# Optimization experiments

Measured on AMD Instinct MI355X. Metric: run time of the kernel, lower is better.

The kernel has to match this reference:

```python
import jax, jax.numpy as jnp
import numpy as np

NUM_HEADS = 8
DIM = 256  # == out_dim; module implicitly requires dim == out_dim


def setup_inputs() -> dict:
    key = jax.random.key(0)
    k0, k1, k2, k3, k4, k5 = jax.random.split(key, 6)
    B, N, T, dim = 4, 128, 128, DIM
    s = dim ** -0.5
    return {
        "v": jax.random.normal(k0, (B, N, T, dim), dtype=jnp.float32),
        "Wq": jax.random.normal(k1, (dim, dim), dtype=jnp.float32) * s,
        "Wk": jax.random.normal(k2, (dim, dim), dtype=jnp.float32) * s,
        "Wv": jax.random.normal(k3, (dim, dim), dtype=jnp.float32) * s,
        "Wp": jax.random.normal(k4, (dim, dim), dtype=jnp.float32) * s,
        "bp": jax.random.normal(k5, (dim,), dtype=jnp.float32) * 0.01,
    }


def reference(v, Wq, Wk, Wv, Wp, bp):
    B, N, T, dim = v.shape
    H = NUM_HEADS
    hd = dim // H
    scale = hd ** -0.5
    # projections (qkv_bias=False)
    q = (v @ Wq).reshape(B * N, T, H, hd)
    k = (v @ Wk).reshape(B * N, T, H, hd)
    vv = (v @ Wv).reshape(B * N, T, H, hd)
    # NOTE: heads axis is NOT moved before the matmul in the original torch
    # code, so attention is over the HEADS axis: per (b*n, t) an HxH matrix.
    attn = jnp.einsum('mthd,mtgd->mthg', q, k) * scale  # [B*N, T, H, H]
    attn = jax.nn.softmax(attn, axis=-1)
    x = jnp.einsum('mthg,mtgd->mthd', attn, vv).reshape(B, N, T, dim)
    # output projection (with bias); dropout probs are 0 / eval mode
    return x @ Wp + bp
```

## Files before the change

### kernel.cpp

```cpp
#include <hip/hip_runtime.h>
#include <hip/hip_bf16.h>
#include <math.h>


#define DIMX      256
#define NH        8
#define HD        32
#define TM        32
#define NTHREADS  512
#define QSTRIDE   776
#define KT        8
#define NT_QKV    48

typedef _Float16 f16x8 __attribute__((ext_vector_type(8)));
typedef _Float16 f16x4 __attribute__((ext_vector_type(4)));
typedef _Float16 f16x2 __attribute__((ext_vector_type(2)));
typedef float    f32x4 __attribute__((ext_vector_type(4)));

static __device__ __forceinline__ f16x2 pkrtz(float a, float b) {
    return (f16x2)__builtin_amdgcn_cvt_pkrtz(a, b);
}

__global__ void pack_weights(const float* __restrict__ Wq,
                             const float* __restrict__ Wk,
                             const float* __restrict__ Wv,
                             const float* __restrict__ Wp,
                             _Float16* __restrict__ pk)
{
    const int QKV_FRAGS = NT_QKV * KT * 64;
    int u = blockIdx.x * blockDim.x + threadIdx.x;
    const float* W;
    int nt, kt, lane;
    if (u < QKV_FRAGS) {
        nt = u / (KT * 64); kt = (u / 64) % KT; lane = u % 64;
        if (nt < 16)      { W = Wq; }
        else if (nt < 32) { W = Wk; nt -= 16; }
        else              { W = Wv; nt -= 32; }
    } else {
        int u2 = u - QKV_FRAGS;
        nt = u2 / (KT * 64); kt = (u2 / 64) % KT; lane = u2 % 64;
        W = Wp;
    }
    const int n  = nt * 16 + (lane & 15);
    const int k0 = kt * 32 + (lane >> 4) * 8;
    f16x8 frag;
#pragma unroll
    for (int j = 0; j < 8; ++j)
        frag[j] = (_Float16)W[(size_t)(k0 + j) * DIMX + n];
    *(f16x8*)(pk + (size_t)u * 8) = frag;
}

__global__ __launch_bounds__(NTHREADS, 6)
void fused_attn_mfma(const float* __restrict__ v,
                     const _Float16* __restrict__ Wqkv_pk,
                     const _Float16* __restrict__ Wp_pk,
                     const float* __restrict__ bp,
                     float* __restrict__ out)
{
    __shared__ __align__(16) _Float16 S[TM * QSTRIDE];

    const int tid   = threadIdx.x;
    const int lane  = tid & 63;
    const int wv_id = tid >> 6;
    const int l15   = lane & 15;
    const int quad  = lane >> 4;
    const long token0 = (long)blockIdx.x * TM;

    {
        const float4* src = (const float4*)(v + token0 * DIMX);
#pragma unroll
        for (int i = 0; i < 4; ++i) {
            int u = tid + NTHREADS * i;
            int m = u >> 6;
            int c = (u & 63) * 4;
            float4 t4 = src[u];
            f16x2 lo = pkrtz(t4.x, t4.y), hi = pkrtz(t4.z, t4.w);
            f16x4 b4 = { lo.x, lo.y, hi.x, hi.y };
            *(f16x4*)&S[m * QSTRIDE + c] = b4;
        }
    }
    __syncthreads();

    f32x4 acc1[2][3];
    int tiles1[3] = { 2 * wv_id, 2 * wv_id + 1, 40 + wv_id };
    {
        int tiles0[3] = { 16 + wv_id * 3, 17 + wv_id * 3, 18 + wv_id * 3 };

        f32x4 acc0[2][3];
#pragma unroll
        for (int tt = 0; tt < 2; ++tt)
#pragma unroll
            for (int j = 0; j < 3; ++j)
                acc0[tt][j] = (f32x4){0.f, 0.f, 0.f, 0.f};
        {
            const f16x8* wb = (const f16x8*)Wqkv_pk + lane;
            f16x8 wcur[3];
#pragma unroll
            for (int j = 0; j < 3; ++j)
                wcur[j] = wb[(size_t)(tiles0[j] * KT) * 64];
            for (int kt = 0; kt < KT; ++kt) {
                const int ktn = (kt + 1 < KT) ? kt + 1 : KT - 1;
                f16x8 wnxt[3];
#pragma unroll
                for (int j = 0; j < 3; ++j)
                    wnxt[j] = wb[(size_t)(tiles0[j] * KT + ktn) * 64];
                f16x8 vf[2];
#pragma unroll
                for (int tt = 0; tt < 2; ++tt)
                    vf[tt] = *(const f16x8*)&S[(tt * 16 + l15) * QSTRIDE + kt * 32 + quad * 8];
#pragma unroll
                for (int j = 0; j < 3; ++j) {
                    acc0[0][j] = __builtin_amdgcn_mfma_f32_16x16x32_f16(wcur[j], vf[0], acc0[0][j], 0, 0, 0);
                    acc0[1][j] = __builtin_amdgcn_mfma_f32_16x16x32_f16(wcur[j], vf[1], acc0[1][j], 0, 0, 0);
                }
#pragma unroll
                for (int j = 0; j < 3; ++j) wcur[j] = wnxt[j];
            }
        }
#pragma unroll
        for (int tt = 0; tt < 2; ++tt)
#pragma unroll
            for (int j = 0; j < 3; ++j) {
                f16x2 a = pkrtz(acc0[tt][j][0], acc0[tt][j][1]);
                f16x2 b = pkrtz(acc0[tt][j][2], acc0[tt][j][3]);
                f16x4 p4 = { a.x, a.y, b.x, b.y };
                *(f16x4*)&S[(tt * 16 + l15) * QSTRIDE + tiles0[j] * 16 + quad * 4] = p4;
            }

#pragma unroll
        for (int tt = 0; tt < 2; ++tt)
#pragma unroll
            for (int j = 0; j < 3; ++j)
                acc1[tt][j] = (f32x4){0.f, 0.f, 0.f, 0.f};
        {
            const f16x8* wb = (const f16x8*)Wqkv_pk + lane;
            f16x8 wcur[3];
#pragma unroll
            for (int j = 0; j < 3; ++j)
                wcur[j] = wb[(size_t)(tiles1[j] * KT) * 64];
            for (int kt = 0; kt < KT; ++kt) {
                const int ktn = (kt + 1 < KT) ? kt + 1 : KT - 1;
                f16x8 wnxt[3];
#pragma unroll
                for (int j = 0; j < 3; ++j)
                    wnxt[j] = wb[(size_t)(tiles1[j] * KT + ktn) * 64];
                f16x8 vf[2];
#pragma unroll
                for (int tt = 0; tt < 2; ++tt)
                    vf[tt] = *(const f16x8*)&S[(tt * 16 + l15) * QSTRIDE + kt * 32 + quad * 8];
#pragma unroll
                for (int j = 0; j < 3; ++j) {
                    acc1[0][j] = __builtin_amdgcn_mfma_f32_16x16x32_f16(wcur[j], vf[0], acc1[0][j], 0, 0, 0);
                    acc1[1][j] = __builtin_amdgcn_mfma_f32_16x16x32_f16(wcur[j], vf[1], acc1[1][j], 0, 0, 0);
                }
#pragma unroll
                for (int j = 0; j < 3; ++j) wcur[j] = wnxt[j];
            }
        }
    }
    __syncthreads();

#pragma unroll
    for (int tt = 0; tt < 2; ++tt)
#pragma unroll
        for (int j = 0; j < 3; ++j) {
            f16x2 a = pkrtz(acc1[tt][j][0], acc1[tt][j][1]);
            f16x2 b = pkrtz(acc1[tt][j][2], acc1[tt][j][3]);
            f16x4 p4 = { a.x, a.y, b.x, b.y };
            *(f16x4*)&S[(tt * 16 + l15) * QSTRIDE + tiles1[j] * 16 + quad * 4] = p4;
        }
    __syncthreads();

    {
        const int ta  = tid >> 4;
        const int sub = tid & 15;
        const int h   = sub >> 1;
        const int d0  = (sub & 1) * 16;
        const float scale = 0.17677669529663687f;

        const _Float16* qrow  = &S[ta * QSTRIDE + h * HD + d0];
        const _Float16* kbase = &S[ta * QSTRIDE + 256 + d0];
        const _Float16* vbase = &S[ta * QSTRIDE + 512 + d0];

        f16x8 q0 = *(const f16x8*)qrow;
        f16x8 q1 = *(const f16x8*)(qrow + 8);

        float logits[NH];
#pragma unroll
        for (int g = 0; g < NH; ++g) {
            f16x8 k0 = *(const f16x8*)(kbase + g * HD);
            f16x8 k1 = *(const f16x8*)(kbase + g * HD + 8);
            f16x8 p  = q0 * k0;
            p += q1 * k1;
            f16x4 r4 = __builtin_shufflevector(p, p, 0, 1, 2, 3)
                     + __builtin_shufflevector(p, p, 4, 5, 6, 7);
            f16x2 r2 = __builtin_shufflevector(r4, r4, 0, 1)
                     + __builtin_shufflevector(r4, r4, 2, 3);
            logits[g] = (float)r2.x + (float)r2.y;
        }
#pragma unroll
        for (int g = 0; g < NH; ++g)
            logits[g] = (logits[g] + __shfl_xor(logits[g], 1, 64)) * scale;

        float mx = logits[0];
#pragma unroll
        for (int g = 1; g < NH; ++g) mx = fmaxf(mx, logits[g]);
        float se = 0.f;
#pragma unroll
        for (int g = 0; g < NH; ++g) { logits[g] = __expf(logits[g] - mx); se += logits[g]; }
        float inv = 1.f / se;

        f16x8 xa0 = (f16x8)(_Float16)0.f;
        f16x8 xa1 = (f16x8)(_Float16)0.f;
#pragma unroll
        for (int g = 0; g < NH; ++g) {
            _Float16 ph = (_Float16)(logits[g] * inv);
            f16x8 pw = { ph, ph, ph, ph, ph, ph, ph, ph };
            f16x8 v0 = *(const f16x8*)(vbase + g * HD);
            f16x8 v1 = *(const f16x8*)(vbase + g * HD + 8);
            xa0 += pw * v0;
            xa1 += pw * v1;
        }
        __syncthreads();
        *(f16x8*)&S[ta * QSTRIDE + h * HD + d0]     = xa0;
        *(f16x8*)&S[ta * QSTRIDE + h * HD + d0 + 8] = xa1;
    }
    __syncthreads();

    {
        const int nt0 = wv_id * 2;
        f32x4 acc[2][2];
#pragma unroll
        for (int tt = 0; tt < 2; ++tt)
#pragma unroll
            for (int j = 0; j < 2; ++j)
                acc[tt][j] = (f32x4){0.f, 0.f, 0.f, 0.f};

        const f16x8* wb = (const f16x8*)Wp_pk + lane;
        f16x8 wcur[2];
#pragma unroll
        for (int j = 0; j < 2; ++j)
            wcur[j] = wb[(size_t)((nt0 + j) * KT) * 64];

        for (int kt = 0; kt < KT; ++kt) {
            const int ktn = (kt + 1 < KT) ? kt + 1 : KT - 1;
            f16x8 wnxt[2];
#pragma unroll
            for (int j = 0; j < 2; ++j)
                wnxt[j] = wb[(size_t)((nt0 + j) * KT + ktn) * 64];
            f16x8 xf[2];
#pragma unroll
            for (int tt = 0; tt < 2; ++tt)
                xf[tt] = *(const f16x8*)&S[(tt * 16 + l15) * QSTRIDE + kt * 32 + quad * 8];
#pragma unroll
            for (int j = 0; j < 2; ++j) {
                acc[0][j] = __builtin_amdgcn_mfma_f32_16x16x32_f16(wcur[j], xf[0], acc[0][j], 0, 0, 0);
                acc[1][j] = __builtin_amdgcn_mfma_f32_16x16x32_f16(wcur[j], xf[1], acc[1][j], 0, 0, 0);
            }
#pragma unroll
            for (int j = 0; j < 2; ++j) wcur[j] = wnxt[j];
        }
#pragma unroll
        for (int j = 0; j < 2; ++j) {
            f32x4 b = *(const f32x4*)&bp[(nt0 + j) * 16 + quad * 4];
#pragma unroll
            for (int tt = 0; tt < 2; ++tt) {
                f32x4 o = acc[tt][j] + b;
                *(f32x4*)&out[(token0 + tt * 16 + l15) * DIMX + (nt0 + j) * 16 + quad * 4] = o;
            }
        }
    }
}

extern "C" void kernel_launch(void* const* d_in, const int* in_sizes, int n_in,
                              void* d_out, int out_size, void* d_ws, size_t ws_size,
                              hipStream_t stream) {
    const float* v  = (const float*)d_in[0];
    const float* Wq = (const float*)d_in[1];
    const float* Wk = (const float*)d_in[2];
    const float* Wv = (const float*)d_in[3];
    const float* Wp = (const float*)d_in[4];
    const float* bp = (const float*)d_in[5];
    float* out = (float*)d_out;

    _Float16* pk = (_Float16*)d_ws;
    const _Float16* Wqkv_pk = pk;
    const _Float16* Wp_pk   = pk + (size_t)24576 * 8;

    pack_weights<<<256, 128, 0, stream>>>(Wq, Wk, Wv, Wp, pk);

    const int ntokens = in_sizes[0] / DIMX;
    fused_attn_mfma<<<ntokens / TM, NTHREADS, 0, stream>>>(v, Wqkv_pk, Wp_pk, bp, out);
}
```

Before: 158.7 us.

## Cache activations in registers and deepen weight prefetch ring for QKV and proj GEMMs

The input tile fragments are loaded from LDS into registers once and reused across all six QKV output tiles. Writes of Q/K/V results to shared memory can then go in place without the two-phase split and its extra barrier. Weight fragments are streamed through an 8-deep register ring (4-deep for the output projection), with Wp prefetch hoisted before the attention stage. The global loads of v and the first weights are also issued before the fp16 conversion. This trades more registers for fewer LDS reads and more latency hiding, and occupancy bounds drop from 6 to 4 waves per SIMD.

```diff
diff --git a/kernel.cpp b/kernel.cpp
--- a/kernel.cpp
+++ b/kernel.cpp
@@ -50,7 +50,7 @@
     *(f16x8*)(pk + (size_t)u * 8) = frag;
 }
 
-__global__ __launch_bounds__(NTHREADS, 6)
+__global__ __launch_bounds__(NTHREADS, 4)
 void fused_attn_mfma(const float* __restrict__ v,
                      const _Float16* __restrict__ Wqkv_pk,
                      const _Float16* __restrict__ Wp_pk,
@@ -66,109 +66,72 @@
     const int quad  = lane >> 4;
     const long token0 = (long)blockIdx.x * TM;
 
-    {
-        const float4* src = (const float4*)(v + token0 * DIMX);
-#pragma unroll
-        for (int i = 0; i < 4; ++i) {
-            int u = tid + NTHREADS * i;
-            int m = u >> 6;
-            int c = (u & 63) * 4;
-            float4 t4 = src[u];
-            f16x2 lo = pkrtz(t4.x, t4.y), hi = pkrtz(t4.z, t4.w);
-            f16x4 b4 = { lo.x, lo.y, hi.x, hi.y };
-            *(f16x4*)&S[m * QSTRIDE + c] = b4;
-        }
-    }
-    __syncthreads();
-
-    f32x4 acc1[2][3];
-    int tiles1[3] = { 2 * wv_id, 2 * wv_id + 1, 40 + wv_id };
-    {
-        int tiles0[3] = { 16 + wv_id * 3, 17 + wv_id * 3, 18 + wv_id * 3 };
-
-        f32x4 acc0[2][3];
-#pragma unroll
-        for (int tt = 0; tt < 2; ++tt)
-#pragma unroll
-            for (int j = 0; j < 3; ++j)
-                acc0[tt][j] = (f32x4){0.f, 0.f, 0.f, 0.f};
-        {
-            const f16x8* wb = (const f16x8*)Wqkv_pk + lane;
-            f16x8 wcur[3];
-#pragma unroll
-            for (int j = 0; j < 3; ++j)
-                wcur[j] = wb[(size_t)(tiles0[j] * KT) * 64];
-            for (int kt = 0; kt < KT; ++kt) {
-                const int ktn = (kt + 1 < KT) ? kt + 1 : KT - 1;
-                f16x8 wnxt[3];
-#pragma unroll
-                for (int j = 0; j < 3; ++j)
-                    wnxt[j] = wb[(size_t)(tiles0[j] * KT + ktn) * 64];
-                f16x8 vf[2];
-#pragma unroll
-                for (int tt = 0; tt < 2; ++tt)
-                    vf[tt] = *(const f16x8*)&S[(tt * 16 + l15) * QSTRIDE + kt * 32 + quad * 8];
-#pragma unroll
-                for (int j = 0; j < 3; ++j) {
-                    acc0[0][j] = __builtin_amdgcn_mfma_f32_16x16x32_f16(wcur[j], vf[0], acc0[0][j], 0, 0, 0);
-                    acc0[1][j] = __builtin_amdgcn_mfma_f32_16x16x32_f16(wcur[j], vf[1], acc0[1][j], 0, 0, 0);
-                }
-#pragma unroll
-                for (int j = 0; j < 3; ++j) wcur[j] = wnxt[j];
+    const int tiles[6] = { 16 + wv_id * 3, 17 + wv_id * 3, 18 + wv_id * 3,
+                           2 * wv_id, 2 * wv_id + 1, 40 + wv_id };
+
+    const float4* src = (const float4*)(v + token0 * DIMX);
+    float4 t4[4];
+#pragma unroll
+    for (int i = 0; i < 4; ++i)
+        t4[i] = src[tid + NTHREADS * i];
+
+    const f16x8* wb = (const f16x8*)Wqkv_pk + lane;
+    f16x8 Wr[8];
+#pragma unroll
+    for (int p = 0; p < 8; ++p)
+        Wr[p] = wb[(size_t)(tiles[0] * KT + p) * 64];
+
+#pragma unroll
+    for (int i = 0; i < 4; ++i) {
+        int u = tid + NTHREADS * i;
+        int m = u >> 6;
+        int c = (u & 63) * 4;
+        f16x2 lo = pkrtz(t4[i].x, t4[i].y), hi = pkrtz(t4[i].z, t4[i].w);
+        f16x4 b4 = { lo.x, lo.y, hi.x, hi.y };
+        *(f16x4*)&S[m * QSTRIDE + c] = b4;
+    }
+    __syncthreads();
+
+    f16x8 vr[2][KT];
+#pragma unroll
+    for (int tt = 0; tt < 2; ++tt)
+#pragma unroll
+        for (int kt = 0; kt < KT; ++kt)
+            vr[tt][kt] = *(const f16x8*)&S[(tt * 16 + l15) * QSTRIDE + kt * 32 + quad * 8];
+    __syncthreads();
+
+#pragma unroll
+    for (int j = 0; j < 6; ++j) {
+        f32x4 acc[2];
+        acc[0] = (f32x4){0.f, 0.f, 0.f, 0.f};
+        acc[1] = (f32x4){0.f, 0.f, 0.f, 0.f};
+#pragma unroll
+        for (int kt = 0; kt < KT; ++kt) {
+            const int u = j * KT + kt;
+            f16x8 w = Wr[u & 7];
+            if (u + 8 < 6 * KT) {
+                const int un = u + 8;
+                Wr[u & 7] = wb[(size_t)(tiles[un >> 3] * KT + (un & 7)) * 64];
             }
-        }
-#pragma unroll
-        for (int tt = 0; tt < 2; ++tt)
-#pragma unroll
-            for (int j = 0; j < 3; ++j) {
-                f16x2 a = pkrtz(acc0[tt][j][0], acc0[tt][j][1]);
-                f16x2 b = pkrtz(acc0[tt][j][2], acc0[tt][j][3]);
-                f16x4 p4 = { a.x, a.y, b.x, b.y };
-                *(f16x4*)&S[(tt * 16 + l15) * QSTRIDE + tiles0[j] * 16 + quad * 4] = p4;
-            }
-
-#pragma unroll
-        for (int tt = 0; tt < 2; ++tt)
-#pragma unroll
-            for (int j = 0; j < 3; ++j)
-                acc1[tt][j] = (f32x4){0.f, 0.f, 0.f, 0.f};
-        {
-            const f16x8* wb = (const f16x8*)Wqkv_pk + lane;
-            f16x8 wcur[3];
-#pragma unroll
-            for (int j = 0; j < 3; ++j)
-                wcur[j] = wb[(size_t)(tiles1[j] * KT) * 64];
-            for (int kt = 0; kt < KT; ++kt) {
-                const int ktn = (kt + 1 < KT) ? kt + 1 : KT - 1;
-                f16x8 wnxt[3];
-#pragma unroll
-                for (int j = 0; j < 3; ++j)
-                    wnxt[j] = wb[(size_t)(tiles1[j] * KT + ktn) * 64];
-                f16x8 vf[2];
-#pragma unroll
-                for (int tt = 0; tt < 2; ++tt)
-                    vf[tt] = *(const f16x8*)&S[(tt * 16 + l15) * QSTRIDE + kt * 32 + quad * 8];
-#pragma unroll
-                for (int j = 0; j < 3; ++j) {
-                    acc1[0][j] = __builtin_amdgcn_mfma_f32_16x16x32_f16(wcur[j], vf[0], acc1[0][j], 0, 0, 0);
-                    acc1[1][j] = __builtin_amdgcn_mfma_f32_16x16x32_f16(wcur[j], vf[1], acc1[1][j], 0, 0, 0);
-                }
-#pragma unroll
-                for (int j = 0; j < 3; ++j) wcur[j] = wnxt[j];
-            }
-        }
-    }
-    __syncthreads();
-
-#pragma unroll
-    for (int tt = 0; tt < 2; ++tt)
-#pragma unroll
-        for (int j = 0; j < 3; ++j) {
-            f16x2 a = pkrtz(acc1[tt][j][0], acc1[tt][j][1]);
-            f16x2 b = pkrtz(acc1[tt][j][2], acc1[tt][j][3]);
+            acc[0] = __builtin_amdgcn_mfma_f32_16x16x32_f16(w, vr[0][kt], acc[0], 0, 0, 0);
+            acc[1] = __builtin_amdgcn_mfma_f32_16x16x32_f16(w, vr[1][kt], acc[1], 0, 0, 0);
+        }
+#pragma unroll
+        for (int tt = 0; tt < 2; ++tt) {
+            f16x2 a = pkrtz(acc[tt][0], acc[tt][1]);
+            f16x2 b = pkrtz(acc[tt][2], acc[tt][3]);
             f16x4 p4 = { a.x, a.y, b.x, b.y };
-            *(f16x4*)&S[(tt * 16 + l15) * QSTRIDE + tiles1[j] * 16 + quad * 4] = p4;
-        }
+            *(f16x4*)&S[(tt * 16 + l15) * QSTRIDE + tiles[j] * 16 + quad * 4] = p4;
+        }
+    }
+
+    const f16x8* wb2 = (const f16x8*)Wp_pk + lane;
+    const int nt0 = wv_id * 2;
+    f16x8 W2[4];
+#pragma unroll
+    for (int p = 0; p < 4; ++p)
+        W2[p] = wb2[(size_t)((nt0 + (p & 1)) * KT + (p >> 1)) * 64];
+
     __syncthreads();
 
     {
@@ -228,7 +191,6 @@
     __syncthreads();
 
     {
-        const int nt0 = wv_id * 2;
         f32x4 acc[2][2];
 #pragma unroll
         for (int tt = 0; tt < 2; ++tt)
@@ -236,29 +198,21 @@
             for (int j = 0; j < 2; ++j)
                 acc[tt][j] = (f32x4){0.f, 0.f, 0.f, 0.f};
 
-        const f16x8* wb = (const f16x8*)Wp_pk + lane;
-        f16x8 wcur[2];
-#pragma unroll
-        for (int j = 0; j < 2; ++j)
-            wcur[j] = wb[(size_t)((nt0 + j) * KT) * 64];
-
+#pragma unroll
         for (int kt = 0; kt < KT; ++kt) {
-            const int ktn = (kt + 1 < KT) ? kt + 1 : KT - 1;
-            f16x8 wnxt[2];
-#pragma unroll
-            for (int j = 0; j < 2; ++j)
-                wnxt[j] = wb[(size_t)((nt0 + j) * KT + ktn) * 64];
             f16x8 xf[2];
 #pragma unroll
             for (int tt = 0; tt < 2; ++tt)
                 xf[tt] = *(const f16x8*)&S[(tt * 16 + l15) * QSTRIDE + kt * 32 + quad * 8];
 #pragma unroll
             for (int j = 0; j < 2; ++j) {
-                acc[0][j] = __builtin_amdgcn_mfma_f32_16x16x32_f16(wcur[j], xf[0], acc[0][j], 0, 0, 0);
-                acc[1][j] = __builtin_amdgcn_mfma_f32_16x16x32_f16(wcur[j], xf[1], acc[1][j], 0, 0, 0);
+                const int u = kt * 2 + j;
+                f16x8 w = W2[u & 3];
+                if (u + 4 < 2 * KT)
+                    W2[u & 3] = wb2[(size_t)((nt0 + j) * KT + (kt + 2)) * 64];
+                acc[0][j] = __builtin_amdgcn_mfma_f32_16x16x32_f16(w, xf[0], acc[0][j], 0, 0, 0);
+                acc[1][j] = __builtin_amdgcn_mfma_f32_16x16x32_f16(w, xf[1], acc[1][j], 0, 0, 0);
             }
-#pragma unroll
-            for (int j = 0; j < 2; ++j) wcur[j] = wnxt[j];
         }
 #pragma unroll
         for (int j = 0; j < 2; ++j) {
```

Result: slower. 254.4 us (+60.3%).

## Enlarge token tile to 48 with deeper weight prefetch and per-head attention threads

Applied to the files above, without the earlier changes.

Raises the per-block token tile from 32 to 48 rows so each weight fragment loaded from global memory feeds three MFMA row tiles instead of two. Adds a two-stage register prefetch of the weight fragments in the fully unrolled k-loops. Reworks the attention phase so each thread handles a whole head without a shuffle reduction, and adds bounds handling for a partial last block. Lowers the launch-bounds occupancy hint from 6 to 2 and uses more LDS per block, which reduces how many blocks fit per CU and leaves some threads idle during attention.

```diff
diff --git a/kernel.cpp b/kernel.cpp
--- a/kernel.cpp
+++ b/kernel.cpp
@@ -6,7 +6,7 @@
 #define DIMX      256
 #define NH        8
 #define HD        32
-#define TM        32
+#define TM        48
 #define NTHREADS  512
 #define QSTRIDE   776
 #define KT        8
@@ -50,12 +50,13 @@
     *(f16x8*)(pk + (size_t)u * 8) = frag;
 }
 
-__global__ __launch_bounds__(NTHREADS, 6)
+__global__ __launch_bounds__(NTHREADS, 2)
 void fused_attn_mfma(const float* __restrict__ v,
                      const _Float16* __restrict__ Wqkv_pk,
                      const _Float16* __restrict__ Wp_pk,
                      const float* __restrict__ bp,
-                     float* __restrict__ out)
+                     float* __restrict__ out,
+                     int ntok)
 {
     __shared__ __align__(16) _Float16 S[TM * QSTRIDE];
 
@@ -64,144 +65,167 @@
     const int wv_id = tid >> 6;
     const int l15   = lane & 15;
     const int quad  = lane >> 4;
-    const long token0 = (long)blockIdx.x * TM;
+    const int token0 = blockIdx.x * TM;
+    int valid = ntok - token0; if (valid > TM) valid = TM;
+
+    const int tiles0[3] = { 16 + 3 * wv_id, 17 + 3 * wv_id, 18 + 3 * wv_id };
+    const int tiles1[3] = { 2 * wv_id, 2 * wv_id + 1, 40 + wv_id };
+
+    const f16x8* wb  = (const f16x8*)Wqkv_pk + lane;
+    const f16x8* wb2 = (const f16x8*)Wp_pk + lane;
 
     {
-        const float4* src = (const float4*)(v + token0 * DIMX);
-#pragma unroll
-        for (int i = 0; i < 4; ++i) {
+        const float4* src = (const float4*)(v + (size_t)token0 * DIMX);
+        float4 t4[6];
+#pragma unroll
+        for (int i = 0; i < 6; ++i) {
+            int u = tid + NTHREADS * i;
+            int m = u >> 6;
+            t4[i] = (m < valid) ? src[u] : (float4){0.f, 0.f, 0.f, 0.f};
+        }
+#pragma unroll
+        for (int i = 0; i < 6; ++i) {
             int u = tid + NTHREADS * i;
             int m = u >> 6;
             int c = (u & 63) * 4;
-            float4 t4 = src[u];
-            f16x2 lo = pkrtz(t4.x, t4.y), hi = pkrtz(t4.z, t4.w);
+            f16x2 lo = pkrtz(t4[i].x, t4[i].y), hi = pkrtz(t4[i].z, t4[i].w);
             f16x4 b4 = { lo.x, lo.y, hi.x, hi.y };
             *(f16x4*)&S[m * QSTRIDE + c] = b4;
         }
     }
-    __syncthreads();
-
-    f32x4 acc1[2][3];
-    int tiles1[3] = { 2 * wv_id, 2 * wv_id + 1, 40 + wv_id };
-    {
-        int tiles0[3] = { 16 + wv_id * 3, 17 + wv_id * 3, 18 + wv_id * 3 };
-
-        f32x4 acc0[2][3];
-#pragma unroll
-        for (int tt = 0; tt < 2; ++tt)
+    f16x8 wA[3], wB[3];
+#pragma unroll
+    for (int j = 0; j < 3; ++j) wA[j] = wb[(size_t)(tiles0[j] * KT + 0) * 64];
+#pragma unroll
+    for (int j = 0; j < 3; ++j) wB[j] = wb[(size_t)(tiles0[j] * KT + 1) * 64];
+    __syncthreads();
+
+    f32x4 acc0[3][3];
+#pragma unroll
+    for (int j = 0; j < 3; ++j)
+#pragma unroll
+        for (int tt = 0; tt < 3; ++tt)
+            acc0[j][tt] = (f32x4){0.f, 0.f, 0.f, 0.f};
+
+#pragma unroll
+    for (int kt = 0; kt < KT; ++kt) {
+        f16x8 wC[3];
+        if (kt < KT - 2) {
 #pragma unroll
             for (int j = 0; j < 3; ++j)
-                acc0[tt][j] = (f32x4){0.f, 0.f, 0.f, 0.f};
-        {
-            const f16x8* wb = (const f16x8*)Wqkv_pk + lane;
-            f16x8 wcur[3];
+                wC[j] = wb[(size_t)(tiles0[j] * KT + kt + 2) * 64];
+        } else {
+#pragma unroll
+            for (int j = 0; j < 3; ++j) wC[j] = wB[j];
+        }
+        f16x8 vf[3];
+#pragma unroll
+        for (int tt = 0; tt < 3; ++tt)
+            vf[tt] = *(const f16x8*)&S[(tt * 16 + l15) * QSTRIDE + kt * 32 + quad * 8];
+#pragma unroll
+        for (int j = 0; j < 3; ++j)
+#pragma unroll
+            for (int tt = 0; tt < 3; ++tt)
+                acc0[j][tt] = __builtin_amdgcn_mfma_f32_16x16x32_f16(wA[j], vf[tt], acc0[j][tt], 0, 0, 0);
+#pragma unroll
+        for (int j = 0; j < 3; ++j) { wA[j] = wB[j]; wB[j] = wC[j]; }
+    }
+
+    f16x8 pA[3], pB[3];
+#pragma unroll
+    for (int j = 0; j < 3; ++j) pA[j] = wb[(size_t)(tiles1[j] * KT + 0) * 64];
+#pragma unroll
+    for (int j = 0; j < 3; ++j) pB[j] = wb[(size_t)(tiles1[j] * KT + 1) * 64];
+
+#pragma unroll
+    for (int j = 0; j < 3; ++j)
+#pragma unroll
+        for (int tt = 0; tt < 3; ++tt) {
+            f16x2 a = pkrtz(acc0[j][tt][0], acc0[j][tt][1]);
+            f16x2 b = pkrtz(acc0[j][tt][2], acc0[j][tt][3]);
+            f16x4 p4 = { a.x, a.y, b.x, b.y };
+            *(f16x4*)&S[(tt * 16 + l15) * QSTRIDE + tiles0[j] * 16 + quad * 4] = p4;
+        }
+
+    f32x4 acc1[3][3];
+#pragma unroll
+    for (int j = 0; j < 3; ++j)
+#pragma unroll
+        for (int tt = 0; tt < 3; ++tt)
+            acc1[j][tt] = (f32x4){0.f, 0.f, 0.f, 0.f};
+
+#pragma unroll
+    for (int kt = 0; kt < KT; ++kt) {
+        f16x8 pC[3];
+        if (kt < KT - 2) {
 #pragma unroll
             for (int j = 0; j < 3; ++j)
-                wcur[j] = wb[(size_t)(tiles0[j] * KT) * 64];
-            for (int kt = 0; kt < KT; ++kt) {
-                const int ktn = (kt + 1 < KT) ? kt + 1 : KT - 1;
-                f16x8 wnxt[3];
-#pragma unroll
-                for (int j = 0; j < 3; ++j)
-                    wnxt[j] = wb[(size_t)(tiles0[j] * KT + ktn) * 64];
-                f16x8 vf[2];
-#pragma unroll
-                for (int tt = 0; tt < 2; ++tt)
-                    vf[tt] = *(const f16x8*)&S[(tt * 16 + l15) * QSTRIDE + kt * 32 + quad * 8];
-#pragma unroll
-                for (int j = 0; j < 3; ++j) {
-                    acc0[0][j] = __builtin_amdgcn_mfma_f32_16x16x32_f16(wcur[j], vf[0], acc0[0][j], 0, 0, 0);
-                    acc0[1][j] = __builtin_amdgcn_mfma_f32_16x16x32_f16(wcur[j], vf[1], acc0[1][j], 0, 0, 0);
-                }
-#pragma unroll
-                for (int j = 0; j < 3; ++j) wcur[j] = wnxt[j];
-            }
-        }
-#pragma unroll
-        for (int tt = 0; tt < 2; ++tt)
-#pragma unroll
-            for (int j = 0; j < 3; ++j) {
-                f16x2 a = pkrtz(acc0[tt][j][0], acc0[tt][j][1]);
-                f16x2 b = pkrtz(acc0[tt][j][2], acc0[tt][j][3]);
-                f16x4 p4 = { a.x, a.y, b.x, b.y };
-                *(f16x4*)&S[(tt * 16 + l15) * QSTRIDE + tiles0[j] * 16 + quad * 4] = p4;
-            }
-
-#pragma unroll
-        for (int tt = 0; tt < 2; ++tt)
-#pragma unroll
-            for (int j = 0; j < 3; ++j)
-                acc1[tt][j] = (f32x4){0.f, 0.f, 0.f, 0.f};
-        {
-            const f16x8* wb = (const f16x8*)Wqkv_pk + lane;
-            f16x8 wcur[3];
-#pragma unroll
-            for (int j = 0; j < 3; ++j)
-                wcur[j] = wb[(size_t)(tiles1[j] * KT) * 64];
-            for (int kt = 0; kt < KT; ++kt) {
-                const int ktn = (kt + 1 < KT) ? kt + 1 : KT - 1;
-                f16x8 wnxt[3];
-#pragma unroll
-                for (int j = 0; j < 3; ++j)
-                    wnxt[j] = wb[(size_t)(tiles1[j] * KT + ktn) * 64];
-                f16x8 vf[2];
-#pragma unroll
-                for (int tt = 0; tt < 2; ++tt)
-                    vf[tt] = *(const f16x8*)&S[(tt * 16 + l15) * QSTRIDE + kt * 32 + quad * 8];
-#pragma unroll
-                for (int j = 0; j < 3; ++j) {
-                    acc1[0][j] = __builtin_amdgcn_mfma_f32_16x16x32_f16(wcur[j], vf[0], acc1[0][j], 0, 0, 0);
-                    acc1[1][j] = __builtin_amdgcn_mfma_f32_16x16x32_f16(wcur[j], vf[1], acc1[1][j], 0, 0, 0);
-                }
-#pragma unroll
-                for (int j = 0; j < 3; ++j) wcur[j] = wnxt[j];
-            }
-        }
-    }
-    __syncthreads();
-
-#pragma unroll
-    for (int tt = 0; tt < 2; ++tt)
-#pragma unroll
-        for (int j = 0; j < 3; ++j) {
-            f16x2 a = pkrtz(acc1[tt][j][0], acc1[tt][j][1]);
-            f16x2 b = pkrtz(acc1[tt][j][2], acc1[tt][j][3]);
+                pC[j] = wb[(size_t)(tiles1[j] * KT + kt + 2) * 64];
+        } else {
+#pragma unroll
+            for (int j = 0; j < 3; ++j) pC[j] = pB[j];
+        }
+        f16x8 vf[3];
+#pragma unroll
+        for (int tt = 0; tt < 3; ++tt)
+            vf[tt] = *(const f16x8*)&S[(tt * 16 + l15) * QSTRIDE + kt * 32 + quad * 8];
+#pragma unroll
+        for (int j = 0; j < 3; ++j)
+#pragma unroll
+            for (int tt = 0; tt < 3; ++tt)
+                acc1[j][tt] = __builtin_amdgcn_mfma_f32_16x16x32_f16(pA[j], vf[tt], acc1[j][tt], 0, 0, 0);
+#pragma unroll
+        for (int j = 0; j < 3; ++j) { pA[j] = pB[j]; pB[j] = pC[j]; }
+    }
+    __syncthreads();
+
+#pragma unroll
+    for (int j = 0; j < 3; ++j)
+#pragma unroll
+        for (int tt = 0; tt < 3; ++tt) {
+            f16x2 a = pkrtz(acc1[j][tt][0], acc1[j][tt][1]);
+            f16x2 b = pkrtz(acc1[j][tt][2], acc1[j][tt][3]);
             f16x4 p4 = { a.x, a.y, b.x, b.y };
             *(f16x4*)&S[(tt * 16 + l15) * QSTRIDE + tiles1[j] * 16 + quad * 4] = p4;
         }
-    __syncthreads();
-
-    {
-        const int ta  = tid >> 4;
-        const int sub = tid & 15;
-        const int h   = sub >> 1;
-        const int d0  = (sub & 1) * 16;
+
+    const int nt0 = 2 * wv_id;
+    f16x8 wA2[2], wB2[2];
+#pragma unroll
+    for (int j = 0; j < 2; ++j) wA2[j] = wb2[(size_t)((nt0 + j) * KT + 0) * 64];
+#pragma unroll
+    for (int j = 0; j < 2; ++j) wB2[j] = wb2[(size_t)((nt0 + j) * KT + 1) * 64];
+    __syncthreads();
+
+    const int ta  = tid >> 3;
+    const int h   = tid & 7;
+    const bool act = (ta < TM);
+    f16x8 xa0, xa1, xa2, xa3;
+    if (act) {
         const float scale = 0.17677669529663687f;
-
-        const _Float16* qrow  = &S[ta * QSTRIDE + h * HD + d0];
-        const _Float16* kbase = &S[ta * QSTRIDE + 256 + d0];
-        const _Float16* vbase = &S[ta * QSTRIDE + 512 + d0];
-
-        f16x8 q0 = *(const f16x8*)qrow;
+        const _Float16* qrow  = &S[ta * QSTRIDE + h * HD];
+        const _Float16* kbase = &S[ta * QSTRIDE + 256];
+        const _Float16* vbase = &S[ta * QSTRIDE + 512];
+
+        f16x8 q0 = *(const f16x8*)(qrow);
         f16x8 q1 = *(const f16x8*)(qrow + 8);
+        f16x8 q2 = *(const f16x8*)(qrow + 16);
+        f16x8 q3 = *(const f16x8*)(qrow + 24);
 
         float logits[NH];
 #pragma unroll
         for (int g = 0; g < NH; ++g) {
-            f16x8 k0 = *(const f16x8*)(kbase + g * HD);
-            f16x8 k1 = *(const f16x8*)(kbase + g * HD + 8);
-            f16x8 p  = q0 * k0;
-            p += q1 * k1;
+            const _Float16* kg = kbase + g * HD;
+            f16x8 p = q0 * *(const f16x8*)(kg);
+            p += q1 * *(const f16x8*)(kg + 8);
+            p += q2 * *(const f16x8*)(kg + 16);
+            p += q3 * *(const f16x8*)(kg + 24);
             f16x4 r4 = __builtin_shufflevector(p, p, 0, 1, 2, 3)
                      + __builtin_shufflevector(p, p, 4, 5, 6, 7);
             f16x2 r2 = __builtin_shufflevector(r4, r4, 0, 1)
                      + __builtin_shufflevector(r4, r4, 2, 3);
-            logits[g] = (float)r2.x + (float)r2.y;
-        }
-#pragma unroll
-        for (int g = 0; g < NH; ++g)
-            logits[g] = (logits[g] + __shfl_xor(logits[g], 1, 64)) * scale;
-
+            logits[g] = ((float)r2.x + (float)r2.y) * scale;
+        }
         float mx = logits[0];
 #pragma unroll
         for (int g = 1; g < NH; ++g) mx = fmaxf(mx, logits[g]);
@@ -210,63 +234,71 @@
         for (int g = 0; g < NH; ++g) { logits[g] = __expf(logits[g] - mx); se += logits[g]; }
         float inv = 1.f / se;
 
-        f16x8 xa0 = (f16x8)(_Float16)0.f;
-        f16x8 xa1 = (f16x8)(_Float16)0.f;
+        xa0 = (f16x8)(_Float16)0.f; xa1 = (f16x8)(_Float16)0.f;
+        xa2 = (f16x8)(_Float16)0.f; xa3 = (f16x8)(_Float16)0.f;
 #pragma unroll
         for (int g = 0; g < NH; ++g) {
             _Float16 ph = (_Float16)(logits[g] * inv);
             f16x8 pw = { ph, ph, ph, ph, ph, ph, ph, ph };
-            f16x8 v0 = *(const f16x8*)(vbase + g * HD);
-            f16x8 v1 = *(const f16x8*)(vbase + g * HD + 8);
-            xa0 += pw * v0;
-            xa1 += pw * v1;
-        }
-        __syncthreads();
-        *(f16x8*)&S[ta * QSTRIDE + h * HD + d0]     = xa0;
-        *(f16x8*)&S[ta * QSTRIDE + h * HD + d0 + 8] = xa1;
+            const _Float16* vg = vbase + g * HD;
+            xa0 += pw * *(const f16x8*)(vg);
+            xa1 += pw * *(const f16x8*)(vg + 8);
+            xa2 += pw * *(const f16x8*)(vg + 16);
+            xa3 += pw * *(const f16x8*)(vg + 24);
+        }
+    }
+    __syncthreads();
+    if (act) {
+        _Float16* xrow = &S[ta * QSTRIDE + h * HD];
+        *(f16x8*)(xrow)      = xa0;
+        *(f16x8*)(xrow + 8)  = xa1;
+        *(f16x8*)(xrow + 16) = xa2;
+        *(f16x8*)(xrow + 24) = xa3;
     }
     __syncthreads();
 
     {
-        const int nt0 = wv_id * 2;
-        f32x4 acc[2][2];
-#pragma unroll
-        for (int tt = 0; tt < 2; ++tt)
+        f32x4 acc2[2][3];
+#pragma unroll
+        for (int j = 0; j < 2; ++j)
+#pragma unroll
+            for (int tt = 0; tt < 3; ++tt)
+                acc2[j][tt] = (f32x4){0.f, 0.f, 0.f, 0.f};
+
+#pragma unroll
+        for (int kt = 0; kt < KT; ++kt) {
+            f16x8 wC2[2];
+            if (kt < KT - 2) {
+#pragma unroll
+                for (int j = 0; j < 2; ++j)
+                    wC2[j] = wb2[(size_t)((nt0 + j) * KT + kt + 2) * 64];
+            } else {
+#pragma unroll
+                for (int j = 0; j < 2; ++j) wC2[j] = wB2[j];
+            }
+            f16x8 xf[3];
+#pragma unroll
+            for (int tt = 0; tt < 3; ++tt)
+                xf[tt] = *(const f16x8*)&S[(tt * 16 + l15) * QSTRIDE + kt * 32 + quad * 8];
 #pragma unroll
             for (int j = 0; j < 2; ++j)
-                acc[tt][j] = (f32x4){0.f, 0.f, 0.f, 0.f};
-
-        const f16x8* wb = (const f16x8*)Wp_pk + lane;
-        f16x8 wcur[2];
-#pragma unroll
-        for (int j = 0; j < 2; ++j)
-            wcur[j] = wb[(size_t)((nt0 + j) * KT) * 64];
-
-        for (int kt = 0; kt < KT; ++kt) {
-            const int ktn = (kt + 1 < KT) ? kt + 1 : KT - 1;
-            f16x8 wnxt[2];
-#pragma unroll
-            for (int j = 0; j < 2; ++j)
-                wnxt[j] = wb[(size_t)((nt0 + j) * KT + ktn) * 64];
-            f16x8 xf[2];
-#pragma unroll
-            for (int tt = 0; tt < 2; ++tt)
-                xf[tt] = *(const f16x8*)&S[(tt * 16 + l15) * QSTRIDE + kt * 32 + quad * 8];
-#pragma unroll
-            for (int j = 0; j < 2; ++j) {
-                acc[0][j] = __builtin_amdgcn_mfma_f32_16x16x32_f16(wcur[j], xf[0], acc[0][j], 0, 0, 0);
-                acc[1][j] = __builtin_amdgcn_mfma_f32_16x16x32_f16(wcur[j], xf[1], acc[1][j], 0, 0, 0);
-            }
-#pragma unroll
-            for (int j = 0; j < 2; ++j) wcur[j] = wnxt[j];
-        }
+#pragma unroll
+                for (int tt = 0; tt < 3; ++tt)
+                    acc2[j][tt] = __builtin_amdgcn_mfma_f32_16x16x32_f16(wA2[j], xf[tt], acc2[j][tt], 0, 0, 0);
+#pragma unroll
+            for (int j = 0; j < 2; ++j) { wA2[j] = wB2[j]; wB2[j] = wC2[j]; }
+        }
+
 #pragma unroll
         for (int j = 0; j < 2; ++j) {
             f32x4 b = *(const f32x4*)&bp[(nt0 + j) * 16 + quad * 4];
 #pragma unroll
-            for (int tt = 0; tt < 2; ++tt) {
-                f32x4 o = acc[tt][j] + b;
-                *(f32x4*)&out[(token0 + tt * 16 + l15) * DIMX + (nt0 + j) * 16 + quad * 4] = o;
+            for (int tt = 0; tt < 3; ++tt) {
+                int row = token0 + tt * 16 + l15;
+                if (row < ntok) {
+                    f32x4 o = acc2[j][tt] + b;
+                    *(f32x4*)&out[(size_t)row * DIMX + (nt0 + j) * 16 + quad * 4] = o;
+                }
             }
         }
     }
@@ -290,5 +322,6 @@
     pack_weights<<<256, 128, 0, stream>>>(Wq, Wk, Wv, Wp, pk);
 
     const int ntokens = in_sizes[0] / DIMX;
-    fused_attn_mfma<<<ntokens / TM, NTHREADS, 0, stream>>>(v, Wqkv_pk, Wp_pk, bp, out);
+    const int nblk = (ntokens + TM - 1) / TM;
+    fused_attn_mfma<<<nblk, NTHREADS, 0, stream>>>(v, Wqkv_pk, Wp_pk, bp, out, ntokens);
 }
```

Measured after the change: 154.9 us. -2.4%, faster.

## Deepen weight prefetch ring across QKV and output GEMM phases

Applied to the files above, without the earlier changes.

Replaces the one-step weight double-buffer with a six-entry register ring fully unrolled over k-tiles. The prefetch carries across the boundary between the two QKV tile groups, and the first output-projection weights are issued before the softmax phase. The weight loads are also issued alongside the initial activation load, so global latency overlaps the fp32-to-fp16 conversion. The aim is to hide global-load latency for weights; the cost is higher register pressure, which may hurt occupancy at 6 waves per SIMD.

```diff
diff --git a/kernel.cpp b/kernel.cpp
--- a/kernel.cpp
+++ b/kernel.cpp
@@ -66,98 +66,105 @@
     const int quad  = lane >> 4;
     const long token0 = (long)blockIdx.x * TM;
 
-    {
-        const float4* src = (const float4*)(v + token0 * DIMX);
-#pragma unroll
-        for (int i = 0; i < 4; ++i) {
-            int u = tid + NTHREADS * i;
-            int m = u >> 6;
-            int c = (u & 63) * 4;
-            float4 t4 = src[u];
-            f16x2 lo = pkrtz(t4.x, t4.y), hi = pkrtz(t4.z, t4.w);
-            f16x4 b4 = { lo.x, lo.y, hi.x, hi.y };
-            *(f16x4*)&S[m * QSTRIDE + c] = b4;
-        }
-    }
-    __syncthreads();
+    const int tiles0[3] = { 16 + wv_id * 3, 17 + wv_id * 3, 18 + wv_id * 3 };
+    const int tiles1[3] = { 2 * wv_id, 2 * wv_id + 1, 40 + wv_id };
+
+    const f16x8* wb  = (const f16x8*)Wqkv_pk + lane;
+    const f16x8* wb2 = (const f16x8*)Wp_pk + lane;
+
+    const float4* src = (const float4*)(v + token0 * DIMX);
+    float4 t4[4];
+#pragma unroll
+    for (int i = 0; i < 4; ++i)
+        t4[i] = src[tid + NTHREADS * i];
+
+    f16x8 Wr[6];
+#pragma unroll
+    for (int p = 0; p < 6; ++p)
+        Wr[p] = wb[(size_t)(tiles0[p % 3] * KT + p / 3) * 64];
+
+#pragma unroll
+    for (int i = 0; i < 4; ++i) {
+        int u = tid + NTHREADS * i;
+        int m = u >> 6;
+        int c = (u & 63) * 4;
+        f16x2 lo = pkrtz(t4[i].x, t4[i].y), hi = pkrtz(t4[i].z, t4[i].w);
+        f16x4 b4 = { lo.x, lo.y, hi.x, hi.y };
+        *(f16x4*)&S[m * QSTRIDE + c] = b4;
+    }
+    __syncthreads();
+
+    f32x4 acc0[2][3];
+#pragma unroll
+    for (int tt = 0; tt < 2; ++tt)
+#pragma unroll
+        for (int j = 0; j < 3; ++j)
+            acc0[tt][j] = (f32x4){0.f, 0.f, 0.f, 0.f};
+
+#pragma unroll
+    for (int kt = 0; kt < KT; ++kt) {
+        f16x8 vf[2];
+#pragma unroll
+        for (int tt = 0; tt < 2; ++tt)
+            vf[tt] = *(const f16x8*)&S[(tt * 16 + l15) * QSTRIDE + kt * 32 + quad * 8];
+#pragma unroll
+        for (int j = 0; j < 3; ++j) {
+            const int u = kt * 3 + j;
+            f16x8 w = Wr[u % 6];
+            if (u + 6 < 24) {
+                const int un = u + 6;
+                Wr[u % 6] = wb[(size_t)(tiles0[un % 3] * KT + un / 3) * 64];
+            } else {
+                const int un = u + 6 - 24;
+                Wr[u % 6] = wb[(size_t)(tiles1[un % 3] * KT + un / 3) * 64];
+            }
+            acc0[0][j] = __builtin_amdgcn_mfma_f32_16x16x32_f16(w, vf[0], acc0[0][j], 0, 0, 0);
+            acc0[1][j] = __builtin_amdgcn_mfma_f32_16x16x32_f16(w, vf[1], acc0[1][j], 0, 0, 0);
+        }
+    }
+
+#pragma unroll
+    for (int tt = 0; tt < 2; ++tt)
+#pragma unroll
+        for (int j = 0; j < 3; ++j) {
+            f16x2 a = pkrtz(acc0[tt][j][0], acc0[tt][j][1]);
+            f16x2 b = pkrtz(acc0[tt][j][2], acc0[tt][j][3]);
+            f16x4 p4 = { a.x, a.y, b.x, b.y };
+            *(f16x4*)&S[(tt * 16 + l15) * QSTRIDE + tiles0[j] * 16 + quad * 4] = p4;
+        }
 
     f32x4 acc1[2][3];
-    int tiles1[3] = { 2 * wv_id, 2 * wv_id + 1, 40 + wv_id };
-    {
-        int tiles0[3] = { 16 + wv_id * 3, 17 + wv_id * 3, 18 + wv_id * 3 };
-
-        f32x4 acc0[2][3];
+#pragma unroll
+    for (int tt = 0; tt < 2; ++tt)
+#pragma unroll
+        for (int j = 0; j < 3; ++j)
+            acc1[tt][j] = (f32x4){0.f, 0.f, 0.f, 0.f};
+
+#pragma unroll
+    for (int kt = 0; kt < KT; ++kt) {
+        f16x8 vf[2];
 #pragma unroll
         for (int tt = 0; tt < 2; ++tt)
-#pragma unroll
-            for (int j = 0; j < 3; ++j)
-                acc0[tt][j] = (f32x4){0.f, 0.f, 0.f, 0.f};
-        {
-            const f16x8* wb = (const f16x8*)Wqkv_pk + lane;
-            f16x8 wcur[3];
-#pragma unroll
-            for (int j = 0; j < 3; ++j)
-                wcur[j] = wb[(size_t)(tiles0[j] * KT) * 64];
-            for (int kt = 0; kt < KT; ++kt) {
-                const int ktn = (kt + 1 < KT) ? kt + 1 : KT - 1;
-                f16x8 wnxt[3];
-#pragma unroll
-                for (int j = 0; j < 3; ++j)
-                    wnxt[j] = wb[(size_t)(tiles0[j] * KT + ktn) * 64];
-                f16x8 vf[2];
-#pragma unroll
-                for (int tt = 0; tt < 2; ++tt)
-                    vf[tt] = *(const f16x8*)&S[(tt * 16 + l15) * QSTRIDE + kt * 32 + quad * 8];
-#pragma unroll
-                for (int j = 0; j < 3; ++j) {
-                    acc0[0][j] = __builtin_amdgcn_mfma_f32_16x16x32_f16(wcur[j], vf[0], acc0[0][j], 0, 0, 0);
-                    acc0[1][j] = __builtin_amdgcn_mfma_f32_16x16x32_f16(wcur[j], vf[1], acc0[1][j], 0, 0, 0);
-                }
-#pragma unroll
-                for (int j = 0; j < 3; ++j) wcur[j] = wnxt[j];
-            }
-        }
-#pragma unroll
-        for (int tt = 0; tt < 2; ++tt)
-#pragma unroll
-            for (int j = 0; j < 3; ++j) {
-                f16x2 a = pkrtz(acc0[tt][j][0], acc0[tt][j][1]);
-                f16x2 b = pkrtz(acc0[tt][j][2], acc0[tt][j][3]);
-                f16x4 p4 = { a.x, a.y, b.x, b.y };
-                *(f16x4*)&S[(tt * 16 + l15) * QSTRIDE + tiles0[j] * 16 + quad * 4] = p4;
-            }
-
-#pragma unroll
-        for (int tt = 0; tt < 2; ++tt)
-#pragma unroll
-            for (int j = 0; j < 3; ++j)
-                acc1[tt][j] = (f32x4){0.f, 0.f, 0.f, 0.f};
-        {
-            const f16x8* wb = (const f16x8*)Wqkv_pk + lane;
-            f16x8 wcur[3];
-#pragma unroll
-            for (int j = 0; j < 3; ++j)
-                wcur[j] = wb[(size_t)(tiles1[j] * KT) * 64];
-            for (int kt = 0; kt < KT; ++kt) {
-                const int ktn = (kt + 1 < KT) ? kt + 1 : KT - 1;
-                f16x8 wnxt[3];
-#pragma unroll
-                for (int j = 0; j < 3; ++j)
-                    wnxt[j] = wb[(size_t)(tiles1[j] * KT + ktn) * 64];
-                f16x8 vf[2];
-#pragma unroll
-                for (int tt = 0; tt < 2; ++tt)
-                    vf[tt] = *(const f16x8*)&S[(tt * 16 + l15) * QSTRIDE + kt * 32 + quad * 8];
-#pragma unroll
-                for (int j = 0; j < 3; ++j) {
-                    acc1[0][j] = __builtin_amdgcn_mfma_f32_16x16x32_f16(wcur[j], vf[0], acc1[0][j], 0, 0, 0);
-                    acc1[1][j] = __builtin_amdgcn_mfma_f32_16x16x32_f16(wcur[j], vf[1], acc1[1][j], 0, 0, 0);
-                }
-#pragma unroll
-                for (int j = 0; j < 3; ++j) wcur[j] = wnxt[j];
-            }
-        }
-    }
+            vf[tt] = *(const f16x8*)&S[(tt * 16 + l15) * QSTRIDE + kt * 32 + quad * 8];
+#pragma unroll
+        for (int j = 0; j < 3; ++j) {
+            const int u = kt * 3 + j;
+            f16x8 w = Wr[u % 6];
+            if (u + 6 < 24) {
+                const int un = u + 6;
+                Wr[u % 6] = wb[(size_t)(tiles1[un % 3] * KT + un / 3) * 64];
+            }
+            acc1[0][j] = __builtin_amdgcn_mfma_f32_16x16x32_f16(w, vf[0], acc1[0][j], 0, 0, 0);
+            acc1[1][j] = __builtin_amdgcn_mfma_f32_16x16x32_f16(w, vf[1], acc1[1][j], 0, 0, 0);
+        }
+    }
+
+    const int nt0 = wv_id * 2;
+    f16x8 W2[4];
+#pragma unroll
+    for (int p = 0; p < 4; ++p)
+        W2[p] = wb2[(size_t)((nt0 + (p & 1)) * KT + (p >> 1)) * 64];
+
     __syncthreads();
 
 #pragma unroll
@@ -228,7 +235,6 @@
     __syncthreads();
 
     {
-        const int nt0 = wv_id * 2;
         f32x4 acc[2][2];
 #pragma unroll
         for (int tt = 0; tt < 2; ++tt)
@@ -236,29 +242,21 @@
             for (int j = 0; j < 2; ++j)
                 acc[tt][j] = (f32x4){0.f, 0.f, 0.f, 0.f};
 
-        const f16x8* wb = (const f16x8*)Wp_pk + lane;
-        f16x8 wcur[2];
-#pragma unroll
-        for (int j = 0; j < 2; ++j)
-            wcur[j] = wb[(size_t)((nt0 + j) * KT) * 64];
-
+#pragma unroll
         for (int kt = 0; kt < KT; ++kt) {
-            const int ktn = (kt + 1 < KT) ? kt + 1 : KT - 1;
-            f16x8 wnxt[2];
-#pragma unroll
-            for (int j = 0; j < 2; ++j)
-                wnxt[j] = wb[(size_t)((nt0 + j) * KT + ktn) * 64];
             f16x8 xf[2];
 #pragma unroll
             for (int tt = 0; tt < 2; ++tt)
                 xf[tt] = *(const f16x8*)&S[(tt * 16 + l15) * QSTRIDE + kt * 32 + quad * 8];
 #pragma unroll
             for (int j = 0; j < 2; ++j) {
-                acc[0][j] = __builtin_amdgcn_mfma_f32_16x16x32_f16(wcur[j], xf[0], acc[0][j], 0, 0, 0);
-                acc[1][j] = __builtin_amdgcn_mfma_f32_16x16x32_f16(wcur[j], xf[1], acc[1][j], 0, 0, 0);
-            }
-#pragma unroll
-            for (int j = 0; j < 2; ++j) wcur[j] = wnxt[j];
+                const int u2 = kt * 2 + j;
+                f16x8 w = W2[u2 % 4];
+                if (u2 + 4 < 16)
+                    W2[u2 % 4] = wb2[(size_t)((nt0 + j) * KT + (kt + 2)) * 64];
+                acc[0][j] = __builtin_amdgcn_mfma_f32_16x16x32_f16(w, xf[0], acc[0][j], 0, 0, 0);
+                acc[1][j] = __builtin_amdgcn_mfma_f32_16x16x32_f16(w, xf[1], acc[1][j], 0, 0, 0);
+            }
         }
 #pragma unroll
         for (int j = 0; j < 2; ++j) {
```

Measured after the change: 170.3 us. 7.3% more time.
